# Kernel tuning notes

Hardware: AMD Instinct MI355X
Metric: run time of the kernel (lower is better)

The kernel has to match this reference:

```python
import jax, jax.numpy as jnp
import numpy as np

N = 50000       # nodes
E = 1600000     # edges (avg degree 32)
DIM = 256       # args.dim (input feature dim)
OUT = 64        # args.n_classes (output dim)
ALPHA = 0.2     # leaky relu negative slope


def setup_inputs() -> dict:
    key = jax.random.key(0)
    k1, k2, k3, k4 = jax.random.split(key, 4)
    x = jax.random.normal(k1, (N, DIM), dtype=jnp.float32)
    # sparse adjacency as COO indices: row 0 = src (output row), row 1 = dst (neighbor)
    edge_index = jax.random.randint(k2, (2, E), 0, N, dtype=jnp.int32)
    # xavier-uniform init as in SpGraphAttentionLayer
    lim_w = float(np.sqrt(6.0 / (DIM + OUT)))
    W = jax.random.uniform(k3, (DIM, OUT), minval=-lim_w, maxval=lim_w, dtype=jnp.float32)
    lim_a = float(np.sqrt(6.0 / (1 + 2 * OUT)))
    a = jax.random.uniform(k4, (2 * OUT,), minval=-lim_a, maxval=lim_a, dtype=jnp.float32)
    return {"x": x, "edge_index": edge_index, "W": W, "a": a}


def reference(x, edge_index, W, a):
    # h = x @ W : [N, OUT]
    h = x @ W
    src = edge_index[0]  # [E] output row index i
    dst = edge_index[1]  # [E] neighbor index j
    # attention logit per edge: a . concat(h[i], h[j])
    logits = h[src] @ a[:OUT] + h[dst] @ a[OUT:]          # [E]
    # edge_e = exp(-leakyrelu(logits))  (note the negation, as in SpGraphAttentionLayer)
    e = jnp.exp(-jax.nn.leaky_relu(logits, ALPHA))         # [E]
    # row-wise normalizer: sum_j e_ij
    rowsum = jax.ops.segment_sum(e, src, num_segments=N)   # [N]
    # aggregated messages: sum_j e_ij * h_j
    agg = jax.ops.segment_sum(e[:, None] * h[dst], src, num_segments=N)  # [N, OUT]
    # h' = agg / rowsum, then elu (concat=True branch)
    return jax.nn.elu(agg / rowsum[:, None])
```

## Files before the change

### kernel.cpp

```cpp
#include <hip/hip_runtime.h>

#define NN 50000
#define NE 1600000
#define DIM 256
#define OUTD 64
#define ALPHA 0.2f

#define BSH 5
#define NB ((NN + 31) >> 5)
#define CAP 1536
#define P1 128
#define EPB (NE / P1)

#define GEMM_BLOCKS ((NN + 63) / 64)
#define WSTRIDE 264
#define ZB 8

typedef unsigned short u16;
typedef unsigned int u32;
typedef __attribute__((ext_vector_type(8))) short short8;
typedef __attribute__((ext_vector_type(4))) float floatx4;

__device__ __forceinline__ u16 f2bf(float f) {
  u32 b = __float_as_uint(f);
  b += 0x7FFFu + ((b >> 16) & 1u);
  return (u16)(b >> 16);
}
__device__ __forceinline__ float bflo(u32 u) { return __uint_as_float(u << 16); }
__device__ __forceinline__ float bfhi(u32 u) { return __uint_as_float(u & 0xFFFF0000u); }

__global__ __launch_bounds__(256) void init_kernel(const float* __restrict__ W,
                                                   u32* __restrict__ wt,
                                                   int* __restrict__ bktcnt) {
  if (blockIdx.x < ZB) {
    const int i = blockIdx.x * 256 + threadIdx.x;
    if (i < NB) bktcnt[i] = 0;
    return;
  }
  const int g = (blockIdx.x - ZB) * 256 + threadIdx.x;
  const int n = g >> 7;
  const int kp = g & 127;
  const float lo = W[(size_t)(2 * kp) * OUTD + n];
  const float hi = W[(size_t)(2 * kp + 1) * OUTD + n];
  wt[g] = (u32)f2bf(lo) | ((u32)f2bf(hi) << 16);
}

__global__ __launch_bounds__(256) void gemm_kernel(
    const float* __restrict__ x, const u32* __restrict__ wt,
    const float* __restrict__ a, u16* __restrict__ hb,
    float* __restrict__ s1, float* __restrict__ s2)
{
  __shared__ u16 Wl[OUTD * WSTRIDE];
  const int t = threadIdx.x;
  {
    const uint4* srcv = (const uint4*)wt;
#pragma unroll
    for (int i = 0; i < 8; ++i) {
      const int c = t + 256 * i;
      const int n = c >> 5;
      const int k8 = c & 31;
      *(uint4*)&Wl[n * WSTRIDE + k8 * 8] = srcv[c];
    }
  }
  __syncthreads();

  const int lane = t & 63;
  const int wv = t >> 6;
  const int n = lane & 15;
  const int quad = lane >> 4;
  int rb = blockIdx.x * 64 + wv * 16;
  if (rb > NN - 16) rb = NN - 16;
  const int row = rb + n;
  const float4* xrow = (const float4*)(x + (size_t)row * DIM);

  floatx4 acc[4] = {{0.f, 0.f, 0.f, 0.f},
                    {0.f, 0.f, 0.f, 0.f},
                    {0.f, 0.f, 0.f, 0.f},
                    {0.f, 0.f, 0.f, 0.f}};

#pragma unroll
  for (int kk = 0; kk < 8; ++kk) {
    const float4 lo = xrow[kk * 8 + quad * 2];
    const float4 hi = xrow[kk * 8 + quad * 2 + 1];
    union { u32 u[4]; short8 s; } af;
    af.u[0] = (u32)f2bf(lo.x) | ((u32)f2bf(lo.y) << 16);
    af.u[1] = (u32)f2bf(lo.z) | ((u32)f2bf(lo.w) << 16);
    af.u[2] = (u32)f2bf(hi.x) | ((u32)f2bf(hi.y) << 16);
    af.u[3] = (u32)f2bf(hi.z) | ((u32)f2bf(hi.w) << 16);
#pragma unroll
    for (int nt = 0; nt < 4; ++nt) {
      const short8 bf =
          *(const short8*)&Wl[(nt * 16 + n) * WSTRIDE + kk * 32 + quad * 8];
      acc[nt] = __builtin_amdgcn_mfma_f32_16x16x32_bf16(af.s, bf, acc[nt], 0, 0, 0);
    }
  }

  float av1[4], av2[4];
#pragma unroll
  for (int nt = 0; nt < 4; ++nt) {
    av1[nt] = a[nt * 16 + n];
    av2[nt] = a[OUTD + nt * 16 + n];
  }

#pragma unroll
  for (int reg = 0; reg < 4; ++reg) {
    const int r = rb + quad * 4 + reg;
    float q1 = acc[0][reg] * av1[0] + acc[1][reg] * av1[1] +
               acc[2][reg] * av1[2] + acc[3][reg] * av1[3];
    float q2 = acc[0][reg] * av2[0] + acc[1][reg] * av2[1] +
               acc[2][reg] * av2[2] + acc[3][reg] * av2[3];
#pragma unroll
    for (int off = 1; off <= 8; off <<= 1) {
      q1 += __shfl_xor(q1, off);
      q2 += __shfl_xor(q2, off);
    }
    if (n == 0) { s1[r] = q1; s2[r] = q2; }
#pragma unroll
    for (int nt = 0; nt < 4; ++nt)
      hb[(size_t)r * OUTD + nt * 16 + n] = f2bf(acc[nt][reg]);
  }
}

__global__ __launch_bounds__(1024) void bin_kernel(
    const int* __restrict__ src, const int* __restrict__ dst,
    int* __restrict__ bktcnt, u32* __restrict__ binned)
{
  __shared__ int lh[NB];
  const int t = threadIdx.x;
  const int p = blockIdx.x;
  for (int i = t; i < NB; i += 1024) lh[i] = 0;
  __syncthreads();

  const int4* src4 = (const int4*)(src + p * EPB);
  const int4* dst4 = (const int4*)(dst + p * EPB);
  for (int i = t; i < EPB / 4; i += 1024) {
    const int4 s = src4[i];
    if ((u32)s.x < (u32)NN) atomicAdd(&lh[s.x >> BSH], 1);
    if ((u32)s.y < (u32)NN) atomicAdd(&lh[s.y >> BSH], 1);
    if ((u32)s.z < (u32)NN) atomicAdd(&lh[s.z >> BSH], 1);
    if ((u32)s.w < (u32)NN) atomicAdd(&lh[s.w >> BSH], 1);
  }
  __syncthreads();

  for (int b = t; b < NB; b += 1024) {
    const int c = lh[b];
    lh[b] = (c > 0) ? atomicAdd(bktcnt + b, c) + b * CAP : 0;
  }
  __syncthreads();

  for (int i = t; i < EPB / 4; i += 1024) {
    const int4 s = src4[i];
    const int4 d = dst4[i];
    int pos, b;
    if ((u32)s.x < (u32)NN) {
      b = s.x >> BSH; pos = atomicAdd(&lh[b], 1);
      if (pos < (b + 1) * CAP) binned[pos] = ((u32)(s.x & 31) << 16) | (u32)(d.x & 0xFFFF);
    }
    if ((u32)s.y < (u32)NN) {
      b = s.y >> BSH; pos = atomicAdd(&lh[b], 1);
      if (pos < (b + 1) * CAP) binned[pos] = ((u32)(s.y & 31) << 16) | (u32)(d.y & 0xFFFF);
    }
    if ((u32)s.z < (u32)NN) {
      b = s.z >> BSH; pos = atomicAdd(&lh[b], 1);
      if (pos < (b + 1) * CAP) binned[pos] = ((u32)(s.z & 31) << 16) | (u32)(d.z & 0xFFFF);
    }
    if ((u32)s.w < (u32)NN) {
      b = s.w >> BSH; pos = atomicAdd(&lh[b], 1);
      if (pos < (b + 1) * CAP) binned[pos] = ((u32)(s.w & 31) << 16) | (u32)(d.w & 0xFFFF);
    }
  }
}

__global__ __launch_bounds__(256) void bucket_agg_kernel(
    const u16* __restrict__ hb, const float* __restrict__ s1,
    const float* __restrict__ s2, const int* __restrict__ bktcnt,
    const u32* __restrict__ binned, float* __restrict__ out)
{
  __shared__ u32 ebuf[CAP];
  __shared__ u16 sdst[CAP];
  __shared__ float wls[CAP];
  __shared__ float s1l[32];
  __shared__ int cnt[32];
  __shared__ int off0[32];
  __shared__ int cur[32];
  const int b = blockIdx.x;
  const int t = threadIdx.x;
  int n = bktcnt[b];
  if (n > CAP) n = CAP;

  if (t < 32) {
    cnt[t] = 0;
    const int nd = b * 32 + t;
    s1l[t] = (nd < NN) ? s1[nd] : 0.f;
  }
  __syncthreads();

  const u32* eb = binned + (size_t)b * CAP;
  for (int i = t; i < n; i += 256) {
    const u32 v = eb[i];
    ebuf[i] = v;
    atomicAdd(&cnt[(v >> 16) & 31], 1);
  }
  __syncthreads();

  if (t < 32) {
    const int v = cnt[t];
    int xx = v;
#pragma unroll
    for (int o = 1; o < 32; o <<= 1) {
      const int y = __shfl_up(xx, o, 32);
      if (t >= o) xx += y;
    }
    off0[t] = xx - v;
    cur[t] = xx - v;
  }
  __syncthreads();

  for (int i = t; i < n; i += 256) {
    const u32 v = ebuf[i];
    const int ln = (v >> 16) & 31;
    const int d = (int)(v & 0xFFFFu);
    const int pos = atomicAdd(&cur[ln], 1);
    sdst[pos] = (u16)d;
    const float logit = s1l[ln] + s2[d];
    const float lr = logit > 0.f ? logit : ALPHA * logit;
    wls[pos] = __expf(-lr);
  }
  __syncthreads();

  const int lane = t & 63;
  const int wv = t >> 6;
  const int g = lane >> 3;
  const int seg = lane & 7;

  for (int ni = 0; ni < 8; ++ni) {
    const int ln = wv * 8 + ni;
    const int node = b * 32 + ln;
    if (node >= NN) continue;
    const int base = off0[ln];
    const int cend = base + cnt[ln];

    float a0 = 0.f, a1 = 0.f, a2 = 0.f, a3 = 0.f;
    float a4 = 0.f, a5 = 0.f, a6 = 0.f, a7 = 0.f;
    float wsum = 0.f;

    for (int e = base + g; e < cend; e += 8) {
      const int dg = sdst[e];
      const float wg = wls[e];
      const uint4 p = *(const uint4*)(hb + (size_t)dg * OUTD + seg * 8);
      a0 = fmaf(wg, bflo(p.x), a0);
      a1 = fmaf(wg, bfhi(p.x), a1);
      a2 = fmaf(wg, bflo(p.y), a2);
      a3 = fmaf(wg, bfhi(p.y), a3);
      a4 = fmaf(wg, bflo(p.z), a4);
      a5 = fmaf(wg, bfhi(p.z), a5);
      a6 = fmaf(wg, bflo(p.w), a6);
      a7 = fmaf(wg, bfhi(p.w), a7);
      wsum += wg;
    }

#pragma unroll
    for (int off = 8; off <= 32; off <<= 1) {
      a0 += __shfl_xor(a0, off);
      a1 += __shfl_xor(a1, off);
      a2 += __shfl_xor(a2, off);
      a3 += __shfl_xor(a3, off);
      a4 += __shfl_xor(a4, off);
      a5 += __shfl_xor(a5, off);
      a6 += __shfl_xor(a6, off);
      a7 += __shfl_xor(a7, off);
      wsum += __shfl_xor(wsum, off);
    }

    if (g == 0) {
      const float inv = (cnt[ln] > 0) ? 1.f / wsum : 0.f;
      float4 r;
      float v;
      v = a0 * inv; r.x = v > 0.f ? v : (__expf(v) - 1.f);
      v = a1 * inv; r.y = v > 0.f ? v : (__expf(v) - 1.f);
      v = a2 * inv; r.z = v > 0.f ? v : (__expf(v) - 1.f);
      v = a3 * inv; r.w = v > 0.f ? v : (__expf(v) - 1.f);
      *(float4*)(out + (size_t)node * OUTD + seg * 8) = r;
      v = a4 * inv; r.x = v > 0.f ? v : (__expf(v) - 1.f);
      v = a5 * inv; r.y = v > 0.f ? v : (__expf(v) - 1.f);
      v = a6 * inv; r.z = v > 0.f ? v : (__expf(v) - 1.f);
      v = a7 * inv; r.w = v > 0.f ? v : (__expf(v) - 1.f);
      *(float4*)(out + (size_t)node * OUTD + seg * 8 + 4) = r;
    }
  }
}

extern "C" void kernel_launch(void* const* d_in, const int* in_sizes, int n_in,
                              void* d_out, int out_size, void* d_ws, size_t ws_size,
                              hipStream_t stream) {
  const float* x = (const float*)d_in[0];
  const int* ei = (const int*)d_in[1];
  const float* W = (const float*)d_in[2];
  const float* a = (const float*)d_in[3];
  float* out = (float*)d_out;

  u16* hb = (u16*)d_ws;
  float* s1 = (float*)(hb + (size_t)NN * OUTD);
  float* s2 = s1 + NN;
  int* bktcnt = (int*)(s2 + NN);
  u32* wt = (u32*)(bktcnt + NB);
  u32* binned = wt + 8192;

  const int* src = ei;
  const int* dst = ei + NE;

  hipLaunchKernelGGL(init_kernel, dim3(ZB + 32), dim3(256), 0, stream,
                     W, wt, bktcnt);
  hipLaunchKernelGGL(gemm_kernel, dim3(GEMM_BLOCKS), dim3(256), 0, stream,
                     x, wt, a, hb, s1, s2);
  hipLaunchKernelGGL(bin_kernel, dim3(P1), dim3(1024), 0, stream,
                     src, dst, bktcnt, binned);
  hipLaunchKernelGGL(bucket_agg_kernel, dim3(NB), dim3(256), 0, stream,
                     hb, s1, s2, bktcnt, binned, out);
}
```

Before: 166.8 us.

## Split bucket counters into per-class sub-buckets and use more binning blocks

Binning now runs on 500 blocks of 256 threads instead of 128 blocks of 1024. Each block belongs to one of 8 classes, and each bucket is split into 8 sub-buckets of 256 slots, one per class. This spreads the global atomicAdd contention on bucket counters across classes and gives more parallelism in the binning pass. The aggregation kernel prefix-sums the per-class counts and compacts the sub-buckets into shared memory. The cost is a higher overflow risk, since each sub-bucket holds 256 entries against an expected average of about 128 per class, plus an extra pass over shared memory.

Result: slower. 193.9 us (+16.3%).

```diff
diff --git a/kernel.cpp b/kernel.cpp
--- a/kernel.cpp
+++ b/kernel.cpp
@@ -8,13 +8,15 @@
 
 #define BSH 5
 #define NB ((NN + 31) >> 5)
-#define CAP 1536
-#define P1 128
+#define NCLS 8
+#define SUBCAP 256
+#define CAP (NCLS * SUBCAP)
+#define P1 500
 #define EPB (NE / P1)
 
 #define GEMM_BLOCKS ((NN + 63) / 64)
 #define WSTRIDE 264
-#define ZB 8
+#define ZB 49
 
 typedef unsigned short u16;
 typedef unsigned int u32;
@@ -34,7 +36,7 @@
                                                    int* __restrict__ bktcnt) {
   if (blockIdx.x < ZB) {
     const int i = blockIdx.x * 256 + threadIdx.x;
-    if (i < NB) bktcnt[i] = 0;
+    if (i < NB * NCLS) bktcnt[i] = 0;
     return;
   }
   const int g = (blockIdx.x - ZB) * 256 + threadIdx.x;
@@ -121,19 +123,20 @@
   }
 }
 
-__global__ __launch_bounds__(1024) void bin_kernel(
+__global__ __launch_bounds__(256) void bin_kernel(
     const int* __restrict__ src, const int* __restrict__ dst,
     int* __restrict__ bktcnt, u32* __restrict__ binned)
 {
   __shared__ int lh[NB];
   const int t = threadIdx.x;
   const int p = blockIdx.x;
-  for (int i = t; i < NB; i += 1024) lh[i] = 0;
+  const int cls = p & (NCLS - 1);
+  for (int i = t; i < NB; i += 256) lh[i] = 0;
   __syncthreads();
 
   const int4* src4 = (const int4*)(src + p * EPB);
   const int4* dst4 = (const int4*)(dst + p * EPB);
-  for (int i = t; i < EPB / 4; i += 1024) {
+  for (int i = t; i < EPB / 4; i += 256) {
     const int4 s = src4[i];
     if ((u32)s.x < (u32)NN) atomicAdd(&lh[s.x >> BSH], 1);
     if ((u32)s.y < (u32)NN) atomicAdd(&lh[s.y >> BSH], 1);
@@ -142,31 +145,37 @@
   }
   __syncthreads();
 
-  for (int b = t; b < NB; b += 1024) {
+  for (int b = t; b < NB; b += 256) {
     const int c = lh[b];
-    lh[b] = (c > 0) ? atomicAdd(bktcnt + b, c) + b * CAP : 0;
-  }
-  __syncthreads();
-
-  for (int i = t; i < EPB / 4; i += 1024) {
+    lh[b] = (c > 0)
+        ? (b * NCLS + cls) * SUBCAP + atomicAdd(bktcnt + b * NCLS + cls, c)
+        : 0;
+  }
+  __syncthreads();
+
+  for (int i = t; i < EPB / 4; i += 256) {
     const int4 s = src4[i];
     const int4 d = dst4[i];
     int pos, b;
     if ((u32)s.x < (u32)NN) {
       b = s.x >> BSH; pos = atomicAdd(&lh[b], 1);
-      if (pos < (b + 1) * CAP) binned[pos] = ((u32)(s.x & 31) << 16) | (u32)(d.x & 0xFFFF);
+      if (pos < (b * NCLS + cls + 1) * SUBCAP)
+        binned[pos] = ((u32)(s.x & 31) << 16) | (u32)(d.x & 0xFFFF);
     }
     if ((u32)s.y < (u32)NN) {
       b = s.y >> BSH; pos = atomicAdd(&lh[b], 1);
-      if (pos < (b + 1) * CAP) binned[pos] = ((u32)(s.y & 31) << 16) | (u32)(d.y & 0xFFFF);
+      if (pos < (b * NCLS + cls + 1) * SUBCAP)
+        binned[pos] = ((u32)(s.y & 31) << 16) | (u32)(d.y & 0xFFFF);
     }
     if ((u32)s.z < (u32)NN) {
       b = s.z >> BSH; pos = atomicAdd(&lh[b], 1);
-      if (pos < (b + 1) * CAP) binned[pos] = ((u32)(s.z & 31) << 16) | (u32)(d.z & 0xFFFF);
+      if (pos < (b * NCLS + cls + 1) * SUBCAP)
+        binned[pos] = ((u32)(s.z & 31) << 16) | (u32)(d.z & 0xFFFF);
     }
     if ((u32)s.w < (u32)NN) {
       b = s.w >> BSH; pos = atomicAdd(&lh[b], 1);
-      if (pos < (b + 1) * CAP) binned[pos] = ((u32)(s.w & 31) << 16) | (u32)(d.w & 0xFFFF);
+      if (pos < (b * NCLS + cls + 1) * SUBCAP)
+        binned[pos] = ((u32)(s.w & 31) << 16) | (u32)(d.w & 0xFFFF);
     }
   }
 }
@@ -179,28 +188,45 @@
   __shared__ u32 ebuf[CAP];
   __shared__ u16 sdst[CAP];
   __shared__ float wls[CAP];
+  __shared__ int coff[NCLS + 1];
   __shared__ float s1l[32];
   __shared__ int cnt[32];
   __shared__ int off0[32];
   __shared__ int cur[32];
   const int b = blockIdx.x;
   const int t = threadIdx.x;
-  int n = bktcnt[b];
-  if (n > CAP) n = CAP;
 
   if (t < 32) {
     cnt[t] = 0;
     const int nd = b * 32 + t;
     s1l[t] = (nd < NN) ? s1[nd] : 0.f;
   }
-  __syncthreads();
-
+  if (t < NCLS) {
+    int c = bktcnt[b * NCLS + t];
+    if (c > SUBCAP) c = SUBCAP;
+    int xx = c;
+#pragma unroll
+    for (int o = 1; o < NCLS; o <<= 1) {
+      const int y = __shfl_up(xx, o, NCLS);
+      if (t >= o) xx += y;
+    }
+    coff[t] = xx - c;
+    if (t == NCLS - 1) coff[NCLS] = xx;
+  }
+  __syncthreads();
+
+  const int n = coff[NCLS];
   const u32* eb = binned + (size_t)b * CAP;
-  for (int i = t; i < n; i += 256) {
-    const u32 v = eb[i];
-    ebuf[i] = v;
-    atomicAdd(&cnt[(v >> 16) & 31], 1);
-  }
+#pragma unroll
+  for (int c = 0; c < NCLS; ++c) {
+    const int base = coff[c];
+    const int nc = coff[c + 1] - base;
+    for (int i = t; i < nc; i += 256) ebuf[base + i] = eb[c * SUBCAP + i];
+  }
+  __syncthreads();
+
+  for (int i = t; i < n; i += 256)
+    atomicAdd(&cnt[(ebuf[i] >> 16) & 31], 1);
   __syncthreads();
 
   if (t < 32) {
@@ -303,7 +329,7 @@
   float* s1 = (float*)(hb + (size_t)NN * OUTD);
   float* s2 = s1 + NN;
   int* bktcnt = (int*)(s2 + NN);
-  u32* wt = (u32*)(bktcnt + NB);
+  u32* wt = (u32*)(bktcnt + NB * NCLS);
   u32* binned = wt + 8192;
 
   const int* src = ei;
@@ -313,7 +339,7 @@
                      W, wt, bktcnt);
   hipLaunchKernelGGL(gemm_kernel, dim3(GEMM_BLOCKS), dim3(256), 0, stream,
                      x, wt, a, hb, s1, s2);
-  hipLaunchKernelGGL(bin_kernel, dim3(P1), dim3(1024), 0, stream,
+  hipLaunchKernelGGL(bin_kernel, dim3(P1), dim3(256), 0, stream,
                      src, dst, bktcnt, binned);
   hipLaunchKernelGGL(bucket_agg_kernel, dim3(NB), dim3(256), 0, stream,
                      hb, s1, s2, bktcnt, binned, out);
```
